# Kernel tuning notes

Measured on AMD Instinct MI355X. Metric: run time of the kernel, lower is better.

Reference implementation:

```python
import jax, jax.numpy as jnp
import numpy as np

D = 384            # d_model
NUM_CLUSTERS = 100
MOM = 0.95         # cluster EMA momentum
ALPHA = 0.02 * (64.0 / D) ** 0.5  # SemanticMemoryLatentSpace alpha schedule
B = 512            # number of items processed sequentially
NORM_CAP = 50.0    # Frobenius-norm saturation threshold


def setup_inputs() -> dict:
    key = jax.random.key(0)
    k1, k2 = jax.random.split(key)
    embeddings = jax.random.normal(k1, (B, D), dtype=jnp.float32)
    # AdaptiveMemoryKernel init: L = randn*0.1 ; K0 = L L^T + 0.1 I (SPD-ish)
    L = jax.random.normal(k2, (D, D), dtype=jnp.float32) * 0.1
    kernel_init = L @ L.T + 0.1 * jnp.eye(D, dtype=jnp.float32)
    return {"embeddings": embeddings, "kernel_init": kernel_init}


def _forward(embeddings, kernel_init):
    def step(carry, e):
        K, prev_norm, count, C, cnts, active = carry
        # --- SemanticNoveltyTracker.compute_novelty: cosine sim vs active centroids ---
        e_norm = jnp.linalg.norm(e)
        c_norms = jnp.linalg.norm(C, axis=1)              # [num_clusters]
        sims = (C @ e) / (c_norms * e_norm + 1e-8)        # vectorized cosine sims
        mask = jnp.arange(NUM_CLUSTERS) < active
        sims_m = jnp.where(mask, sims, -2.0)              # mask inactive clusters
        max_sim = jnp.max(sims_m)
        closest = jnp.argmax(sims_m)
        novelty = jnp.where(active == 0, 1.0, 1.0 - max_sim ** 2)
        novelty = jnp.clip(novelty, 0.0, 1.0)
        # --- AdaptiveMemoryKernel.update_kernel ---
        pert = jnp.outer(e, e)                            # symmetric by construction
        tr = jnp.trace(pert)
        pert = jnp.where(tr > 1e-8, pert / jnp.maximum(tr, 1e-8) * D, pert)
        iw = novelty ** 1.5                               # squared-novelty weighting
        norm_before = jnp.linalg.norm(K)
        growth = jnp.where((count > 0) & (prev_norm > 0),
                           (norm_before - prev_norm) / jnp.maximum(prev_norm, 1e-12), 0.0)
        a = jnp.where(growth < 0.01, ALPHA * 1.5, ALPHA)  # boost when plateauing
        K = K + (a * iw) * pert
        K = (K + K.T) * 0.5                               # symmetrize
        kn = jnp.linalg.norm(K)
        K = jnp.where(kn > NORM_CAP, K / kn * NORM_CAP, K)  # soft saturation clip
        new_norm = jnp.linalg.norm(K)
        # --- SemanticNoveltyTracker.update_cluster ---
        create_new = (novelty > 0.7) & (active < NUM_CLUSTERS)
        idx = jnp.where(create_new, active, closest).astype(jnp.int32)
        old = C[idx]
        newc = jnp.where(create_new, e, MOM * old + (1.0 - MOM) * e)
        C = C.at[idx].set(newc)
        cnts = cnts.at[idx].set(jnp.where(create_new, 1.0, cnts[idx] + 1.0))
        active = active + create_new.astype(jnp.int32)
        return (K, new_norm, count + 1, C, cnts, active), None

    C0 = jnp.zeros((NUM_CLUSTERS, D), dtype=embeddings.dtype)
    cnts0 = jnp.zeros((NUM_CLUSTERS,), dtype=embeddings.dtype)
    init = (kernel_init, jnp.float32(0.0), jnp.int32(0), C0, cnts0, jnp.int32(0))
    (K, _, _, _, _, _), _ = jax.lax.scan(step, init, embeddings)
    # space warping: apply evolved kernel to the batch
    refined = embeddings @ K                              # [B, D]
    return refined


def reference(embeddings, kernel_init):
    return _forward(embeddings, kernel_init)
```

## Files before the change

### kernel.cpp

```cpp
#include <hip/hip_runtime.h>


#define A_BOOSTF 0.012247448713915891f

template <int CTRL>
__device__ __forceinline__ float dpp_f(float x) {
  return __int_as_float(
      __builtin_amdgcn_mov_dpp(__float_as_int(x), CTRL, 0xf, 0xf, true));
}
template <int CTRL>
__device__ __forceinline__ unsigned dpp_u(unsigned x) {
  return (unsigned)__builtin_amdgcn_mov_dpp((int)x, CTRL, 0xf, 0xf, true);
}
__device__ __forceinline__ float rdlane_f(float x, int l) {
  return __int_as_float(__builtin_amdgcn_readlane(__float_as_int(x), l));
}
__device__ __forceinline__ unsigned rdlane_u(unsigned x, int l) {
  return (unsigned)__builtin_amdgcn_readlane((int)x, l);
}
__device__ __forceinline__ float wave_sum64(float v) {
  v += dpp_f<0xB1>(v);
  v += dpp_f<0x4E>(v);
  v += dpp_f<0x124>(v);
  v += dpp_f<0x128>(v);
  return (rdlane_f(v, 0) + rdlane_f(v, 16)) + (rdlane_f(v, 32) + rdlane_f(v, 48));
}
__device__ __forceinline__ unsigned sortable(float v) {
  unsigned u = __float_as_uint(v);
  return u ^ (unsigned)(((int)u >> 31) | 0x80000000);
}
__device__ __forceinline__ float unsortable(unsigned x) {
  unsigned u = (x & 0x80000000u) ? (x ^ 0x80000000u) : ~x;
  return __uint_as_float(u);
}
__device__ __forceinline__ unsigned wave_umax64(unsigned v) {
  v = max(v, dpp_u<0xB1>(v));
  v = max(v, dpp_u<0x4E>(v));
  v = max(v, dpp_u<0x124>(v));
  v = max(v, dpp_u<0x128>(v));
  return max(max(rdlane_u(v, 0), rdlane_u(v, 16)),
             max(rdlane_u(v, 32), rdlane_u(v, 48)));
}

#define GX(D)                                                                  \
  ((D) < 4 ? ((D) == 0   ? gq[0].x                                             \
              : (D) == 1 ? gq[0].y                                             \
              : (D) == 2 ? gq[0].z                                             \
                         : gq[0].w)                                            \
   : (D) < 8                                                                   \
       ? ((D) == 4   ? gq[1].x                                                 \
          : (D) == 5 ? gq[1].y                                                 \
          : (D) == 6 ? gq[1].z                                                 \
                     : gq[1].w)                                                \
   : (D) < 12 ? ((D) == 8    ? gq[2].x                                         \
                 : (D) == 9  ? gq[2].y                                         \
                 : (D) == 10 ? gq[2].z                                         \
                             : gq[2].w)                                        \
              : ((D) == 12   ? gq[3].x                                         \
                 : (D) == 13 ? gq[3].y                                         \
                 : (D) == 14 ? gq[3].z                                         \
                             : gq[3].w))

__global__ __launch_bounds__(256) void gemm_nt(const float* __restrict__ A,
                                               const float* __restrict__ B,
                                               float* __restrict__ C,
                                               int N, int K) {
  __shared__ float As[32][33];
  __shared__ float Bs[32][33];
  int bx = blockIdx.x, by = blockIdx.y;
  int tid = threadIdx.x;
  int tx = tid & 15, ty = tid >> 4;
  float a00 = 0.f, a01 = 0.f, a10 = 0.f, a11 = 0.f;
  for (int k0 = 0; k0 < K; k0 += 32) {
    for (int l = tid; l < 1024; l += 256) {
      int r = l >> 5, c = l & 31;
      As[r][c] = A[(by * 32 + r) * K + k0 + c];
      Bs[r][c] = B[(bx * 32 + r) * K + k0 + c];
    }
    __syncthreads();
#pragma unroll
    for (int k = 0; k < 32; ++k) {
      float x0 = As[2 * ty][k], x1 = As[2 * ty + 1][k];
      float y0 = Bs[2 * tx][k], y1 = Bs[2 * tx + 1][k];
      a00 += x0 * y0; a01 += x0 * y1; a10 += x1 * y0; a11 += x1 * y1;
    }
    __syncthreads();
  }
  int i = by * 32 + 2 * ty, jj = bx * 32 + 2 * tx;
  C[i * N + jj] = a00;           C[i * N + jj + 1] = a01;
  C[(i + 1) * N + jj] = a10;     C[(i + 1) * N + jj + 1] = a11;
}

__global__ __launch_bounds__(256) void gemm_nn(const float* __restrict__ A,
                                               const float* __restrict__ B,
                                               float* __restrict__ C,
                                               int N, int K) {
  __shared__ float As[32][33];
  __shared__ float Bs[32][33];
  int bx = blockIdx.x, by = blockIdx.y;
  int tid = threadIdx.x;
  int tx = tid & 15, ty = tid >> 4;
  float a00 = 0.f, a01 = 0.f, a10 = 0.f, a11 = 0.f;
  for (int k0 = 0; k0 < K; k0 += 32) {
    for (int l = tid; l < 1024; l += 256) {
      int r = l >> 5, c = l & 31;
      As[r][c] = A[(by * 32 + r) * K + k0 + c];
      Bs[r][c] = B[(k0 + r) * N + bx * 32 + c];
    }
    __syncthreads();
#pragma unroll
    for (int k = 0; k < 32; ++k) {
      float x0 = As[2 * ty][k], x1 = As[2 * ty + 1][k];
      float y0 = Bs[k][2 * tx], y1 = Bs[k][2 * tx + 1];
      a00 += x0 * y0; a01 += x0 * y1; a10 += x1 * y0; a11 += x1 * y1;
    }
    __syncthreads();
  }
  int i = by * 32 + 2 * ty, jj = bx * 32 + 2 * tx;
  C[i * N + jj] = a00;           C[i * N + jj + 1] = a01;
  C[(i + 1) * N + jj] = a10;     C[(i + 1) * N + jj + 1] = a11;
}

__global__ __launch_bounds__(256) void final_gemm(const float* __restrict__ G,
                                                  const float* __restrict__ E,
                                                  const float* __restrict__ M0,
                                                  const float* __restrict__ W,
                                                  const float* __restrict__ gS,
                                                  float* __restrict__ out) {
  __shared__ float As[32][33];
  __shared__ float Bs[32][33];
  int bx = blockIdx.x, by = blockIdx.y;
  int tid = threadIdx.x;
  int tx = tid & 15, ty = tid >> 4;
  float a00 = 0.f, a01 = 0.f, a10 = 0.f, a11 = 0.f;
  for (int k0 = 0; k0 < 512; k0 += 32) {
    for (int l = tid; l < 1024; l += 256) {
      int r = l >> 5, c = l & 31;
      As[r][c] = G[(by * 32 + r) * 512 + k0 + c] * W[k0 + c];
      Bs[r][c] = E[(k0 + r) * 384 + bx * 32 + c];
    }
    __syncthreads();
#pragma unroll
    for (int k = 0; k < 32; ++k) {
      float x0 = As[2 * ty][k], x1 = As[2 * ty + 1][k];
      float y0 = Bs[k][2 * tx], y1 = Bs[k][2 * tx + 1];
      a00 += x0 * y0; a01 += x0 * y1; a10 += x1 * y0; a11 += x1 * y1;
    }
    __syncthreads();
  }
  float gv = gS[0];
  int i = by * 32 + 2 * ty, jj = bx * 32 + 2 * tx;
  out[i * 384 + jj]         = gv * M0[i * 384 + jj]         + a00;
  out[i * 384 + jj + 1]     = gv * M0[i * 384 + jj + 1]     + a01;
  out[(i + 1) * 384 + jj]     = gv * M0[(i + 1) * 384 + jj]     + a10;
  out[(i + 1) * 384 + jj + 1] = gv * M0[(i + 1) * 384 + jj + 1] + a11;
}

__global__ __launch_bounds__(256) void prep_kernel(const float* __restrict__ E,
                                                   const float* __restrict__ M0,
                                                   const float* __restrict__ K0,
                                                   float* __restrict__ u,
                                                   float* __restrict__ Kpart) {
  __shared__ double wr[4];
  int b = blockIdx.x;
  int tid = threadIdx.x, lane = tid & 63, wv = tid >> 6;
  if (b < 128) {
    int row = b * 4 + wv;
    const float4* e4 = (const float4*)(E + row * 384);
    const float4* m4 = (const float4*)(M0 + row * 384);
    float p = 0.f;
    for (int i = lane; i < 96; i += 64) {
      float4 a = e4[i], bb = m4[i];
      p += a.x * bb.x + a.y * bb.y + a.z * bb.z + a.w * bb.w;
    }
#pragma unroll
    for (int off = 32; off; off >>= 1) p += __shfl_down(p, off);
    if (lane == 0) u[row] = p;
  } else {
    int cb = b - 128;
    const float* p = K0 + cb * 2304 + tid * 9;
    double acc = 0.0;
#pragma unroll
    for (int i = 0; i < 9; ++i) { double v = (double)p[i]; acc += v * v; }
#pragma unroll
    for (int off = 32; off; off >>= 1) acc += __shfl_down(acc, off);
    if (lane == 0) wr[wv] = acc;
    __syncthreads();
    if (tid == 0) Kpart[cb] = (float)(wr[0] + wr[1] + wr[2] + wr[3]);
  }
}

__global__ __launch_bounds__(192) void scan_kernel(const float* __restrict__ G,
                                                   const float* __restrict__ u,
                                                   const float* __restrict__ Kpart,
                                                   float* __restrict__ Wout,
                                                   float* __restrict__ gOut) {
  __shared__ float RAW[100 * 257];
  __shared__ float gx_tbl[512 * 16];
  __shared__ float ren_tbl[512];
  __shared__ float u_sh[512];
  __shared__ float wh_sh[512];
  __shared__ float RG_bnew[512];
  __shared__ float RG_nov[512];
  __shared__ int RG_idx[512];
  __shared__ int FLAG;
  __shared__ int FLAG2;

  const int tid = threadIdx.x;
  const int wid = tid >> 6;
  const int lane = tid & 63;

  float4 z4 = {0.f, 0.f, 0.f, 0.f};
  for (int i = tid; i < 6425; i += 192) ((float4*)RAW)[i] = z4;
  for (int tt = tid; tt < 512; tt += 192) {
    const float* gr = G + tt * 512 + tt;
    const int lim = 512 - tt;
#pragma unroll
    for (int d = 0; d < 16; ++d)
      gx_tbl[tt * 16 + d] = (d < lim) ? gr[d] : 0.f;
    ren_tbl[tt] = __builtin_amdgcn_rcpf(__builtin_amdgcn_sqrtf(gr[0]));
  }
  if (tid < 128) ((float4*)u_sh)[tid] = ((const float4*)u)[tid];
  if (tid == 0) { FLAG = 0; FLAG2 = -1; }
  __syncthreads();

  if (wid == 0) {
    float d0 = 1.f, d1 = 1.f, cn0 = 0.f, cn1 = 0.f, s0 = 0.f, s1 = 0.f;
    int nact = 0;
    float r0[8], r1[8];
#pragma unroll
    for (int j = 0; j < 8; ++j) { r0[j] = 0.f; r1[j] = 0.f; }

    const float4* gx4 = (const float4*)gx_tbl;
    float4 gq[4];
    float renk;
    gq[0] = gx4[0]; gq[1] = gx4[1]; gq[2] = gx4[2]; gq[3] = gx4[3];
    renk = ren_tbl[0];

#define W0STEP(K)                                                              \
    {                                                                          \
                                \
      const int tnx = (t + (K) + 1 < 512) ? t + (K) + 1 : 511;                 \
      float4 gqn0 = gx4[tnx * 4], gqn1 = gx4[tnx * 4 + 1];                     \
      float4 gqn2 = gx4[tnx * 4 + 2], gqn3 = gx4[tnx * 4 + 3];                 \
      float renn = ren_tbl[tnx];                                               \
      const float trk = gq[0].x;                                               \
      float v0 = (lane < nact) ? s0 * renk * r0[K] : -2.f;                     \
      float v1 = (lane + 64 < nact) ? s1 * renk * r1[K] : -2.f;                \
      unsigned pk0 = (sortable(v0) & ~127u) | (unsigned)(127 - lane);          \
      unsigned pk1 = (sortable(v1) & ~127u) | (unsigned)(63 - lane);           \
      unsigned P = wave_umax64(max(pk0, pk1));                                 \
      int imax = 127 - (int)(P & 127u);                                        \
      float M = unsortable(P & ~127u);                                         \
      float nov = (nact == 0) ? 1.f : fminf(1.f, fmaxf(0.f, 1.f - M * M));     \
      int create = (nov > 0.7f && nact < 100) ? 1 : 0;                         \
      const int idxs = create ? nact : imax;                                   \
      const int cl = idxs & 63, hi = idxs >> 6;                                \
      float dcA = create ? 1.f : 0.95f * d0;                                   \
      float dcB = create ? 1.f : 0.95f * d1;                                   \
      float ccA = create ? trk                                                 \
                         : (0.9025f * cn0 + 0.095f * (d0 * r0[K]) +            \
                            0.0025f * trk);                                    \
      float ccB = create ? trk                                                 \
                         : (0.9025f * cn1 + 0.095f * (d1 * r1[K]) +            \
                            0.0025f * trk);                                    \
      float scA = dcA * __builtin_amdgcn_rcpf(__builtin_amdgcn_sqrtf(ccA));    \
      float scB = dcB * __builtin_amdgcn_rcpf(__builtin_amdgcn_sqrtf(ccB));    \
      float ivA = 0.05f * __builtin_amdgcn_rcpf(dcA);                          \
      float ivB = 0.05f * __builtin_amdgcn_rcpf(dcB);                          \
      bool own0 = (lane == cl) && (hi == 0);                                   \
      bool own1 = (lane == cl) && (hi == 1);                                   \
      d0 = own0 ? dcA : d0; cn0 = own0 ? ccA : cn0; s0 = own0 ? scA : s0;      \
      d1 = own1 ? dcB : d1; cn1 = own1 ? ccB : cn1; s1 = own1 ? scB : s1;      \
      float bnew = create ? 1.f : rdlane_f(hi ? ivB : ivA, cl);                \
      nact += create;                                                          \
      float pb0 = own0 ? bnew : 0.f, pb1 = own1 ? bnew : 0.f;                  \
      _Pragma("unroll") for (int j = (K) + 1; j < 8; ++j) {                    \
        r0[j] += pb0 * GX((j) - (K));                                          \
        r1[j] += pb1 * GX((j) - (K));                                          \
      }                                                                        \
      _Pragma("unroll") for (int j = 0; j < 8; ++j) {                          \
        pa0[j] += pb0 * GX(8 + (j) - (K));                                     \
        pa1[j] += pb1 * GX(8 + (j) - (K));                                     \
      }                                                                        \
      bnewA[K] = bnew; novA[K] = nov; idxA[K] = idxs;                          \
      gq[0] = gqn0; gq[1] = gqn1; gq[2] = gqn2; gq[3] = gqn3;                  \
      renk = renn;                                                             \
    }

    for (int R = 0; R < 64; ++R) {
      const int t = 8 * R;
      const int tn = t + 8;
      const int cnx = tn & 255;

      if (t == 256) {
        while (__hip_atomic_load(&FLAG2, __ATOMIC_ACQUIRE,
                                 __HIP_MEMORY_SCOPE_WORKGROUP) < 31)
          __builtin_amdgcn_s_sleep(1);
        for (int i = lane; i < 6425; i += 64) ((float4*)RAW)[i] = z4;
        __builtin_amdgcn_sched_barrier(0);
        const float* Gb = G + 256;
        float A[4][4], Bv[4][4];
        float ab[4], bb[4];
        int ai[4], bi[4];
#pragma unroll
        for (int j = 0; j < 4; ++j) {
#pragma unroll
          for (int m = 0; m < 4; ++m) A[j][m] = Gb[j * 512 + m * 64 + lane];
          ab[j] = RG_bnew[j]; ai[j] = RG_idx[j];
        }
        for (int s = 0; s < 256; s += 8) {
#pragma unroll
          for (int j = 0; j < 4; ++j) {
#pragma unroll
            for (int m = 0; m < 4; ++m)
              Bv[j][m] = Gb[(s + 4 + j) * 512 + m * 64 + lane];
            bb[j] = RG_bnew[s + 4 + j]; bi[j] = RG_idx[s + 4 + j];
          }
#pragma unroll
          for (int j = 0; j < 4; ++j) {
#pragma unroll
            for (int m = 0; m < 4; ++m) {
              const int a_ = ai[j] * 257 + m * 64 + lane;
              RAW[a_] += ab[j] * A[j][m];
            }
          }
          if (s + 8 < 256) {
#pragma unroll
            for (int j = 0; j < 4; ++j) {
#pragma unroll
              for (int m = 0; m < 4; ++m)
                A[j][m] = Gb[(s + 8 + j) * 512 + m * 64 + lane];
              ab[j] = RG_bnew[s + 8 + j]; ai[j] = RG_idx[s + 8 + j];
            }
          }
#pragma unroll
          for (int j = 0; j < 4; ++j) {
#pragma unroll
            for (int m = 0; m < 4; ++m) {
              const int a_ = bi[j] * 257 + m * 64 + lane;
              RAW[a_] += bb[j] * Bv[j][m];
            }
          }
        }
        __builtin_amdgcn_sched_barrier(0);
#pragma unroll
        for (int j = 0; j < 8; ++j) r0[j] = RAW[lane * 257 + j];
        if (lane < 36) {
#pragma unroll
          for (int j = 0; j < 8; ++j) r1[j] = RAW[(lane + 64) * 257 + j];
        }
        __builtin_amdgcn_sched_barrier(0);
      }

      float bnewA[8], novA[8];
      int idxA[8];
      float pa0[8], pa1[8];
#pragma unroll
      for (int j = 0; j < 8; ++j) { pa0[j] = 0.f; pa1[j] = 0.f; }

      W0STEP(0) W0STEP(1) W0STEP(2) W0STEP(3)
      W0STEP(4) W0STEP(5) W0STEP(6) W0STEP(7)

      if (tn < 512 && cnx != 0) {
        while (__hip_atomic_load(&FLAG2, __ATOMIC_ACQUIRE,
                                 __HIP_MEMORY_SCOPE_WORKGROUP) < R - 1)
          __builtin_amdgcn_s_sleep(1);
        float r0n[8], r1n[8];
#pragma unroll
        for (int j = 0; j < 8; ++j) r0n[j] = RAW[lane * 257 + cnx + j];
        if (lane < 36) {
#pragma unroll
          for (int j = 0; j < 8; ++j) r1n[j] = RAW[(lane + 64) * 257 + cnx + j];
        } else {
#pragma unroll
          for (int j = 0; j < 8; ++j) r1n[j] = 0.f;
        }
#pragma unroll
        for (int j = 0; j < 8; ++j) {
          r0[j] = r0n[j] + pa0[j];
          r1[j] = r1n[j] + pa1[j];
        }
      }
      __builtin_amdgcn_sched_barrier(0);

      if (lane == 0) {
#pragma unroll
        for (int k = 0; k < 8; ++k) {
          RG_bnew[t + k] = bnewA[k];
          RG_nov[t + k] = novA[k];
          RG_idx[t + k] = idxA[k];
        }
        __hip_atomic_store(&FLAG, R + 1, __ATOMIC_RELEASE,
                           __HIP_MEMORY_SCOPE_WORKGROUP);
      }
    }
#undef W0STEP
  } else if (wid == 1) {
    for (int r = 0; r < 64; ++r) {
      const int t = 8 * r;
      const int c = t & 255;
      const int gbase = (t >> 6) & ~3;

      float B4[8][4];
#pragma unroll
      for (int k = 0; k < 8; ++k)
#pragma unroll
        for (int mg = 0; mg < 4; ++mg)
          B4[k][mg] = G[(t + k) * 512 + (gbase + mg) * 64 + lane];

      while (__hip_atomic_load(&FLAG, __ATOMIC_ACQUIRE,
                               __HIP_MEMORY_SCOPE_WORKGROUP) < r + 1)
        __builtin_amdgcn_s_sleep(1);

      float bn[8];
      int id[8];
#pragma unroll
      for (int k = 0; k < 8; ++k) { bn[k] = RG_bnew[t + k]; id[k] = RG_idx[t + k]; }

#pragma unroll
      for (int k = 0; k < 8; ++k) {
#pragma unroll
        for (int mg = 0; mg < 4; ++mg)
          if (mg * 64 + 63 >= c) {
            const int a_ = id[k] * 257 + mg * 64 + lane;
            RAW[a_] += bn[k] * B4[k][mg];
          }
      }
      __hip_atomic_store(&FLAG2, r, __ATOMIC_RELEASE,
                         __HIP_MEMORY_SCOPE_WORKGROUP);
    }
  } else {
    float q8[8];
#pragma unroll
    for (int gI = 0; gI < 8; ++gI) q8[gI] = 0.f;
    float n2 = wave_sum64(Kpart[lane]);
    float g = 1.f, ginv = 1.f;

    for (int r = 0; r < 64; ++r) {
      const int t = 8 * r;
      float B[8][8];
#pragma unroll
      for (int k = 0; k < 8; ++k)
#pragma unroll
        for (int gI = 0; gI < 8; ++gI)
          B[k][gI] = G[(t + k) * 512 + gI * 64 + lane];

      while (__hip_atomic_load(&FLAG, __ATOMIC_ACQUIRE,
                               __HIP_MEMORY_SCOPE_WORKGROUP) < r + 1)
        __builtin_amdgcn_s_sleep(1);

      float novv[8];
#pragma unroll
      for (int k = 0; k < 8; ++k) novv[k] = RG_nov[t + k];

      float trm[8], gxw[8][8];
#pragma unroll
      for (int m = 0; m < 8; ++m) {
        trm[m] = gx_tbl[(t + m) * 16];
#pragma unroll
        for (int j = m + 1; j < 8; ++j)
          gxw[m][j] = gx_tbl[(t + m) * 16 + (j - m)];
      }
      float4 uuA = *(const float4*)&u_sh[t];
      float4 uuB = *(const float4*)&u_sh[t + 4];
      float um[8] = {uuA.x, uuA.y, uuA.z, uuA.w, uuB.x, uuB.y, uuB.z, uuB.w};

      const int grp = t >> 6;
      float qsel = q8[0];
#pragma unroll
      for (int gI = 1; gI < 8; ++gI) qsel = (grp == gI) ? q8[gI] : qsel;
      float qeff[8];
#pragma unroll
      for (int k = 0; k < 8; ++k) qeff[k] = rdlane_f(qsel, (t & 63) + k);

      float wh[8];
#pragma unroll
      for (int m = 0; m < 8; ++m) {
        float nov = novv[m];
        float iw = nov * __builtin_amdgcn_sqrtf(nov);
        float psc = 384.0f * __builtin_amdgcn_rcpf(fmaxf(trm[m], 1e-8f));
        float ccf = A_BOOSTF * iw * psc;
        float qv = g * (um[m] + qeff[m]);
        float n2n = n2 + 2.f * ccf * qv + ccf * ccf * trm[m] * trm[m];
        float kn = __builtin_amdgcn_sqrtf(n2n);
        float fct = (kn > 50.f) ? 50.f * __builtin_amdgcn_rcpf(kn) : 1.f;
        float fiv = (kn > 50.f) ? kn * 0.02f : 1.f;
        wh[m] = ccf * ginv;
        n2 = n2n * fct * fct; g *= fct; ginv *= fiv;
#pragma unroll
        for (int j = m + 1; j < 8; ++j)
          qeff[j] += wh[m] * gxw[m][j] * gxw[m][j];
      }

      if (lane == 0) {
#pragma unroll
        for (int m = 0; m < 8; ++m) wh_sh[t + m] = wh[m];
      }
#pragma unroll
      for (int gI = 0; gI < 8; ++gI)
#pragma unroll
        for (int k = 0; k < 8; ++k)
          q8[gI] += wh[k] * B[k][gI] * B[k][gI];
    }

    for (int s2 = lane; s2 < 512; s2 += 64) Wout[s2] = wh_sh[s2] * g;
    if (lane == 0) gOut[0] = g;
  }
}

extern "C" void kernel_launch(void* const* d_in, const int* in_sizes, int n_in,
                              void* d_out, int out_size, void* d_ws,
                              size_t ws_size, hipStream_t stream) {
  const float* E = (const float*)d_in[0];
  const float* K0 = (const float*)d_in[1];
  float* out = (float*)d_out;

  float* G = (float*)d_ws;
  float* M0 = G + 512 * 512;
  float* u = M0 + 512 * 384;
  float* W = u + 512;
  float* gS = W + 512;
  float* Kpart = gS + 1;

  gemm_nt<<<dim3(16, 16), 256, 0, stream>>>(E, E, G, 512, 384);
  gemm_nn<<<dim3(12, 16), 256, 0, stream>>>(E, K0, M0, 384, 384);
  prep_kernel<<<192, 256, 0, stream>>>(E, M0, K0, u, Kpart);
  scan_kernel<<<1, 192, 0, stream>>>(G, u, Kpart, W, gS);
  final_gemm<<<dim3(12, 16), 256, 0, stream>>>(G, E, M0, W, gS, out);
}
```

Baseline: 259.8 us.

## Offload midpoint RAW rebuild to helper waves and overlap LDS reads with steps

The serial wave 0 used to zero and rebuild the 100x257 RAW cluster-accumulator table at step 256 by itself. That rebuild now goes to the helper waves, split by cluster index into two halves (below and at-or-above 50), and each half signals completion through new FLAG3A/FLAG3B flags. The RAW prefetch for the next round is moved to sit between steps 4 and 7 so its LDS latency is hidden behind compute, and wave 0 gets a higher scheduling priority. The risk is that the helper waves' own loops are delayed by this work and the flag handshakes add extra synchronization.

```diff
diff --git a/kernel.cpp b/kernel.cpp
--- a/kernel.cpp
+++ b/kernel.cpp
@@ -205,6 +205,8 @@
   __shared__ int RG_idx[512];
   __shared__ int FLAG;
   __shared__ int FLAG2;
+  __shared__ int FLAG3A;
+  __shared__ int FLAG3B;
 
   const int tid = threadIdx.x;
   const int wid = tid >> 6;
@@ -221,10 +223,11 @@
     ren_tbl[tt] = __builtin_amdgcn_rcpf(__builtin_amdgcn_sqrtf(gr[0]));
   }
   if (tid < 128) ((float4*)u_sh)[tid] = ((const float4*)u)[tid];
-  if (tid == 0) { FLAG = 0; FLAG2 = -1; }
+  if (tid == 0) { FLAG = 0; FLAG2 = -1; FLAG3A = 0; FLAG3B = 0; }
   __syncthreads();
 
   if (wid == 0) {
+    __builtin_amdgcn_s_setprio(1);
     float d0 = 1.f, d1 = 1.f, cn0 = 0.f, cn1 = 0.f, s0 = 0.f, s1 = 0.f;
     int nact = 0;
     float r0[8], r1[8];
@@ -239,7 +242,6 @@
 
 #define W0STEP(K)                                                              \
     {                                                                          \
-                                \
       const int tnx = (t + (K) + 1 < 512) ? t + (K) + 1 : 511;                 \
       float4 gqn0 = gx4[tnx * 4], gqn1 = gx4[tnx * 4 + 1];                     \
       float4 gqn2 = gx4[tnx * 4 + 2], gqn3 = gx4[tnx * 4 + 3];                 \
@@ -294,56 +296,12 @@
       const int cnx = tn & 255;
 
       if (t == 256) {
-        while (__hip_atomic_load(&FLAG2, __ATOMIC_ACQUIRE,
-                                 __HIP_MEMORY_SCOPE_WORKGROUP) < 31)
+        while (__hip_atomic_load(&FLAG3A, __ATOMIC_ACQUIRE,
+                                 __HIP_MEMORY_SCOPE_WORKGROUP) == 0)
           __builtin_amdgcn_s_sleep(1);
-        for (int i = lane; i < 6425; i += 64) ((float4*)RAW)[i] = z4;
-        __builtin_amdgcn_sched_barrier(0);
-        const float* Gb = G + 256;
-        float A[4][4], Bv[4][4];
-        float ab[4], bb[4];
-        int ai[4], bi[4];
-#pragma unroll
-        for (int j = 0; j < 4; ++j) {
-#pragma unroll
-          for (int m = 0; m < 4; ++m) A[j][m] = Gb[j * 512 + m * 64 + lane];
-          ab[j] = RG_bnew[j]; ai[j] = RG_idx[j];
-        }
-        for (int s = 0; s < 256; s += 8) {
-#pragma unroll
-          for (int j = 0; j < 4; ++j) {
-#pragma unroll
-            for (int m = 0; m < 4; ++m)
-              Bv[j][m] = Gb[(s + 4 + j) * 512 + m * 64 + lane];
-            bb[j] = RG_bnew[s + 4 + j]; bi[j] = RG_idx[s + 4 + j];
-          }
-#pragma unroll
-          for (int j = 0; j < 4; ++j) {
-#pragma unroll
-            for (int m = 0; m < 4; ++m) {
-              const int a_ = ai[j] * 257 + m * 64 + lane;
-              RAW[a_] += ab[j] * A[j][m];
-            }
-          }
-          if (s + 8 < 256) {
-#pragma unroll
-            for (int j = 0; j < 4; ++j) {
-#pragma unroll
-              for (int m = 0; m < 4; ++m)
-                A[j][m] = Gb[(s + 8 + j) * 512 + m * 64 + lane];
-              ab[j] = RG_bnew[s + 8 + j]; ai[j] = RG_idx[s + 8 + j];
-            }
-          }
-#pragma unroll
-          for (int j = 0; j < 4; ++j) {
-#pragma unroll
-            for (int m = 0; m < 4; ++m) {
-              const int a_ = bi[j] * 257 + m * 64 + lane;
-              RAW[a_] += bb[j] * Bv[j][m];
-            }
-          }
-        }
-        __builtin_amdgcn_sched_barrier(0);
+        while (__hip_atomic_load(&FLAG3B, __ATOMIC_ACQUIRE,
+                                 __HIP_MEMORY_SCOPE_WORKGROUP) == 0)
+          __builtin_amdgcn_s_sleep(1);
 #pragma unroll
         for (int j = 0; j < 8; ++j) r0[j] = RAW[lane * 257 + j];
         if (lane < 36) {
@@ -360,13 +318,13 @@
       for (int j = 0; j < 8; ++j) { pa0[j] = 0.f; pa1[j] = 0.f; }
 
       W0STEP(0) W0STEP(1) W0STEP(2) W0STEP(3)
-      W0STEP(4) W0STEP(5) W0STEP(6) W0STEP(7)
-
-      if (tn < 512 && cnx != 0) {
+
+      float r0n[8], r1n[8];
+      const bool doRead = (tn < 512) && (cnx != 0);
+      if (doRead) {
         while (__hip_atomic_load(&FLAG2, __ATOMIC_ACQUIRE,
                                  __HIP_MEMORY_SCOPE_WORKGROUP) < R - 1)
           __builtin_amdgcn_s_sleep(1);
-        float r0n[8], r1n[8];
 #pragma unroll
         for (int j = 0; j < 8; ++j) r0n[j] = RAW[lane * 257 + cnx + j];
         if (lane < 36) {
@@ -376,6 +334,11 @@
 #pragma unroll
           for (int j = 0; j < 8; ++j) r1n[j] = 0.f;
         }
+      }
+
+      W0STEP(4) W0STEP(5) W0STEP(6) W0STEP(7)
+
+      if (doRead) {
 #pragma unroll
         for (int j = 0; j < 8; ++j) {
           r0[j] = r0n[j] + pa0[j];
@@ -429,6 +392,37 @@
       }
       __hip_atomic_store(&FLAG2, r, __ATOMIC_RELEASE,
                          __HIP_MEMORY_SCOPE_WORKGROUP);
+
+      if (r == 31) {
+        for (int i = lane; i < 3212; i += 64) ((float4*)RAW)[i] = z4;
+        if (lane < 2) RAW[12848 + lane] = 0.f;
+        __builtin_amdgcn_sched_barrier(0);
+        const float* Gb = G + 256;
+        for (int s = 0; s < 256; s += 4) {
+          float A[4][4], bh[4];
+          int idj[4];
+#pragma unroll
+          for (int j = 0; j < 4; ++j) {
+            bh[j] = RG_bnew[s + j]; idj[j] = RG_idx[s + j];
+#pragma unroll
+            for (int m = 0; m < 4; ++m)
+              A[j][m] = Gb[(s + j) * 512 + m * 64 + lane];
+          }
+#pragma unroll
+          for (int j = 0; j < 4; ++j) {
+            if (idj[j] < 50) {
+#pragma unroll
+              for (int m = 0; m < 4; ++m) {
+                const int a_ = idj[j] * 257 + m * 64 + lane;
+                RAW[a_] += bh[j] * A[j][m];
+              }
+            }
+          }
+        }
+        __builtin_amdgcn_sched_barrier(0);
+        __hip_atomic_store(&FLAG3A, 1, __ATOMIC_RELEASE,
+                           __HIP_MEMORY_SCOPE_WORKGROUP);
+      }
     }
   } else {
     float q8[8];
@@ -439,6 +433,41 @@
 
     for (int r = 0; r < 64; ++r) {
       const int t = 8 * r;
+
+      if (r == 32) {
+        while (__hip_atomic_load(&FLAG2, __ATOMIC_ACQUIRE,
+                                 __HIP_MEMORY_SCOPE_WORKGROUP) < 31)
+          __builtin_amdgcn_s_sleep(1);
+        if (lane < 2) RAW[12850 + lane] = 0.f;
+        for (int i = 3213 + lane; i < 6425; i += 64) ((float4*)RAW)[i] = z4;
+        __builtin_amdgcn_sched_barrier(0);
+        const float* Gb = G + 256;
+        for (int s = 0; s < 256; s += 4) {
+          float A[4][4], bh[4];
+          int idj[4];
+#pragma unroll
+          for (int j = 0; j < 4; ++j) {
+            bh[j] = RG_bnew[s + j]; idj[j] = RG_idx[s + j];
+#pragma unroll
+            for (int m = 0; m < 4; ++m)
+              A[j][m] = Gb[(s + j) * 512 + m * 64 + lane];
+          }
+#pragma unroll
+          for (int j = 0; j < 4; ++j) {
+            if (idj[j] >= 50) {
+#pragma unroll
+              for (int m = 0; m < 4; ++m) {
+                const int a_ = idj[j] * 257 + m * 64 + lane;
+                RAW[a_] += bh[j] * A[j][m];
+              }
+            }
+          }
+        }
+        __builtin_amdgcn_sched_barrier(0);
+        __hip_atomic_store(&FLAG3B, 1, __ATOMIC_RELEASE,
+                           __HIP_MEMORY_SCOPE_WORKGROUP);
+      }
+
       float B[8][8];
 #pragma unroll
       for (int k = 0; k < 8; ++k)
```

Result: slower. 275.6 us (+6.1%).
